# Kernel optimization log

Measured on AMD Instinct MI355X. Metric: run time of the kernel, lower is better.

The kernel has to match this reference:

```python
import jax, jax.numpy as jnp
import numpy as np

N_QUBITS = 12
N_LAYERS = 16
DIM = 1 << N_QUBITS        # 4096
BATCH = 2048
N_CLASS = 5                # Z observables on wires 0..4

# --- static circuit structure (qubit 0 = most significant bit, DeepQuantum order) ---
_idx = np.arange(DIM)

def _cnot_perm(c, t):
    # CNOT(control=c, target=t): flip target bit where control bit is 1
    cbit = 1 << (N_QUBITS - 1 - c)
    tbit = 1 << (N_QUBITS - 1 - t)
    return np.where(_idx & cbit, _idx ^ tbit, _idx)

# cnot_ring: CNOT(q, (q+1) % n) for q = 0..n-1
CNOT_PERMS = [jnp.asarray(_cnot_perm(q, (q + 1) % N_QUBITS)) for q in range(N_QUBITS)]

# <Z_w> sign vectors for wires 0..4, stacked to (N_CLASS, DIM)
Z_SIGNS = jnp.asarray(
    np.stack([1.0 - 2.0 * ((_idx >> (N_QUBITS - 1 - w)) & 1) for w in range(N_CLASS)]).astype(np.float32)
)


def _apply_ry(psi, theta, q):
    """Apply RY(theta) on qubit q to batched state psi of shape (B, DIM)."""
    c = jnp.cos(theta / 2).astype(psi.real.dtype)
    s = jnp.sin(theta / 2).astype(psi.real.dtype)
    b = psi.shape[0]
    psi = psi.reshape(b, 1 << q, 2, 1 << (N_QUBITS - 1 - q))
    p0, p1 = psi[:, :, 0, :], psi[:, :, 1, :]
    out = jnp.stack([c * p0 - s * p1, s * p0 + c * p1], axis=2)
    return out.reshape(b, DIM)


def _circuit(psi, thetas):
    """num_layers x (RY layer + CNOT ring); returns (B, N_CLASS) Z expectations."""
    for l in range(N_LAYERS):
        for q in range(N_QUBITS):
            psi = _apply_ry(psi, thetas[l, q], q)
        for q in range(N_QUBITS):
            psi = psi[:, CNOT_PERMS[q]]
    probs = psi.real * psi.real + psi.imag * psi.imag  # (B, DIM)
    return probs @ Z_SIGNS.T                           # (B, N_CLASS)


def setup_inputs() -> dict:
    key = jax.random.key(0)
    k1, k2, k3, k4 = jax.random.split(key, 4)
    zr = jax.random.normal(k1, (BATCH, DIM), dtype=jnp.float32)
    zi = jax.random.normal(k2, (BATCH, DIM), dtype=jnp.float32)
    norm = jnp.sqrt(jnp.sum(zr * zr + zi * zi, axis=1, keepdims=True))  # valid quantum state
    zr, zi = zr / norm, zi / norm
    thetas = jax.random.normal(k3, (N_LAYERS, N_QUBITS), dtype=jnp.float32)
    y = jax.random.randint(k4, (BATCH,), 0, N_CLASS, dtype=jnp.int64)
    return {"z_real": zr, "z_imag": zi, "thetas": thetas, "y": y}


def reference(z_real, z_imag, thetas, y):
    psi = jax.lax.complex(z_real, z_imag)              # (B, 2**n) complex64
    output = _circuit(psi, thetas)                     # (B, N_CLASS) float32
    logp = jax.nn.log_softmax(output, axis=-1)
    nll = -jnp.take_along_axis(logp, y[:, None].astype(jnp.int32), axis=1)[:, 0]
    loss = jnp.mean(nll)                               # F.cross_entropy(output, y)
    return (loss, output)
```

## Files before the change

kernel.cpp:

```cpp
#include <hip/hip_runtime.h>
#include <math.h>


#define DIM     4096
#define NLAYERS 16
#define BATCH   2048
#define NCLASS  5

typedef float v2f __attribute__((ext_vector_type(2)));

__host__ __device__ constexpr unsigned gperm(unsigned i) {
  for (int q = 11; q >= 0; --q) {
    const unsigned cbit = 1u << (11 - q);
    const unsigned tbit = 1u << (11 - ((q + 1) % 12));
    if (i & cbit) i ^= tbit;
  }
  return i;
}
__host__ __device__ constexpr unsigned Qmap(unsigned lo) {
  return ((lo ^ (lo >> 3)) & 1u) | ((((lo >> 1) ^ (lo >> 3)) & 1u) << 1) |
         (((lo >> 2) & 1u) << 2) | ((lo & 1u) << 3);
}
__host__ __device__ constexpr unsigned Fmap(unsigned x) {
  return (x & 0xF00u) | ((x & 0xFu) << 4) | (((x >> 4) & 0xFu) ^ Qmap(x & 0xFu));
}

#define FOR16(M) M(0) M(1) M(2) M(3) M(4) M(5) M(6) M(7) M(8) M(9) M(10) \
  M(11) M(12) M(13) M(14) M(15)

#define ROT(i, j) {                                          \
    const v2f ti = p##i, tj = p##j;                          \
    p##i = __builtin_elementwise_fma(nkv, tj, ti);           \
    p##j = __builtin_elementwise_fma(kv,  ti, tj); }

#define GM8 ROT(0,8) ROT(1,9) ROT(2,10) ROT(3,11) ROT(4,12) ROT(5,13) \
  ROT(6,14) ROT(7,15)
#define GM4 ROT(0,4) ROT(1,5) ROT(2,6) ROT(3,7) ROT(8,12) ROT(9,13) \
  ROT(10,14) ROT(11,15)
#define GM2 ROT(0,2) ROT(1,3) ROT(4,6) ROT(5,7) ROT(8,10) ROT(9,11) \
  ROT(12,14) ROT(13,15)
#define GM1 ROT(0,1) ROT(2,3) ROT(4,5) ROT(6,7) ROT(8,9) ROT(10,11) \
  ROT(12,13) ROT(14,15)

#define GETK(g) \
  const float kG = __int_as_float(__builtin_amdgcn_readlane( \
      __float_as_int(vkg[(g) & 3]), l + (((g) >> 2) << 4)));

#define DPP8(CTRL, iA,iB,iC,iD,iE,iF,iG,iH) { \
    float a0 = p##iA.x, a1 = p##iA.y, a2 = p##iB.x, a3 = p##iB.y, \
          a4 = p##iC.x, a5 = p##iC.y, a6 = p##iD.x, a7 = p##iD.y, \
          a8 = p##iE.x, a9 = p##iE.y, a10 = p##iF.x, a11 = p##iF.y, \
          a12 = p##iG.x, a13 = p##iG.y, a14 = p##iH.x, a15 = p##iH.y; \
    asm("s_nop 1\n\t" \
        "v_fmac_f32_dpp %0, %0, %16 " CTRL "\n\t" \
        "v_fmac_f32_dpp %1, %1, %16 " CTRL "\n\t" \
        "v_fmac_f32_dpp %2, %2, %16 " CTRL "\n\t" \
        "v_fmac_f32_dpp %3, %3, %16 " CTRL "\n\t" \
        "v_fmac_f32_dpp %4, %4, %16 " CTRL "\n\t" \
        "v_fmac_f32_dpp %5, %5, %16 " CTRL "\n\t" \
        "v_fmac_f32_dpp %6, %6, %16 " CTRL "\n\t" \
        "v_fmac_f32_dpp %7, %7, %16 " CTRL "\n\t" \
        "v_fmac_f32_dpp %8, %8, %16 " CTRL "\n\t" \
        "v_fmac_f32_dpp %9, %9, %16 " CTRL "\n\t" \
        "v_fmac_f32_dpp %10, %10, %16 " CTRL "\n\t" \
        "v_fmac_f32_dpp %11, %11, %16 " CTRL "\n\t" \
        "v_fmac_f32_dpp %12, %12, %16 " CTRL "\n\t" \
        "v_fmac_f32_dpp %13, %13, %16 " CTRL "\n\t" \
        "v_fmac_f32_dpp %14, %14, %16 " CTRL "\n\t" \
        "v_fmac_f32_dpp %15, %15, %16 " CTRL \
        : "+v"(a0), "+v"(a1), "+v"(a2), "+v"(a3), "+v"(a4), "+v"(a5), \
          "+v"(a6), "+v"(a7), "+v"(a8), "+v"(a9), "+v"(a10), "+v"(a11), \
          "+v"(a12), "+v"(a13), "+v"(a14), "+v"(a15) \
        : "v"(sg)); \
    p##iA.x = a0;  p##iA.y = a1;  p##iB.x = a2;  p##iB.y = a3; \
    p##iC.x = a4;  p##iC.y = a5;  p##iD.x = a6;  p##iD.y = a7; \
    p##iE.x = a8;  p##iE.y = a9;  p##iF.x = a10; p##iF.y = a11; \
    p##iG.x = a12; p##iG.y = a13; p##iH.x = a14; p##iH.y = a15; }

#define DPPGATE(CTRL) \
  DPP8(CTRL, 0,1,2,3,4,5,6,7) DPP8(CTRL, 8,9,10,11,12,13,14,15)

__global__ __launch_bounds__(256)
void qnn_sim(const float* __restrict__ zr, const float* __restrict__ zi,
             const float* __restrict__ thetas, const int* __restrict__ y,
             float* __restrict__ out) {
  __shared__ v2f buf2[DIM];
  const int b = blockIdx.x;
  const int t = threadIdx.x;

  const int tn = t ^ (((t >> 2) & 1) * 3);

  const int w1b = ((t & 0xF0) << 4) | (tn & 0xF);
  const int r1b = (int)Fmap((unsigned)t);
  const int Gtn = ((tn << 4) ^ (tn << 3)) & 0xFFF;
  const int r2b = (int)Fmap((unsigned)Gtn);

#define MKADDR(i) \
  const int w1a##i = w1b ^ (int)Fmap((unsigned)i); \
  const int r2a##i = r2b ^ (int)Fmap(gperm((unsigned)i));
  FOR16(MKADDR)
#undef MKADDR

  const bool m7 = ((t ^ (t >> 2)) & 1) != 0;
  const bool m6 = (((t >> 1) ^ (t >> 2)) & 1) != 0;
  const bool m5 = ((t >> 2) & 1) != 0;
  const bool m4 = ((t >> 3) & 1) != 0;

  v2f p0,p1,p2,p3,p4,p5,p6,p7,p8,p9,p10,p11,p12,p13,p14,p15;
  {
    const float4* zr4 = (const float4*)(zr + (size_t)b * DIM + (tn << 4));
    const float4* zi4 = (const float4*)(zi + (size_t)b * DIM + (tn << 4));
    const float4 a0 = zr4[0], a1 = zr4[1], a2 = zr4[2], a3 = zr4[3];
    const float4 b0 = zi4[0], b1 = zi4[1], b2 = zi4[2], b3 = zi4[3];
    p0  = (v2f){a0.x, b0.x}; p1  = (v2f){a0.y, b0.y};
    p2  = (v2f){a0.z, b0.z}; p3  = (v2f){a0.w, b0.w};
    p4  = (v2f){a1.x, b1.x}; p5  = (v2f){a1.y, b1.y};
    p6  = (v2f){a1.z, b1.z}; p7  = (v2f){a1.w, b1.w};
    p8  = (v2f){a2.x, b2.x}; p9  = (v2f){a2.y, b2.y};
    p10 = (v2f){a2.z, b2.z}; p11 = (v2f){a2.w, b2.w};
    p12 = (v2f){a3.x, b3.x}; p13 = (v2f){a3.y, b3.y};
    p14 = (v2f){a3.z, b3.z}; p15 = (v2f){a3.w, b3.w};
  }

  float vkg[4];
  {
    const int lane = t & 63;
    if (lane < 48) {
      const int lsrc = lane & 15;
      const int gb = (lane >> 4) << 2;
#pragma unroll
      for (int j = 0; j < 4; ++j) {
        const float a = 0.5f * thetas[lsrc * 12 + gb + j];
        vkg[j] = sinf(a) / cosf(a);
      }
    } else {
      const int lsrc = lane - 48;
      float c = 1.f;
      for (int g = 0; g < 12; ++g) c *= cosf(0.5f * thetas[lsrc * 12 + g]);
      vkg[0] = c; vkg[1] = 0.f; vkg[2] = 0.f; vkg[3] = 0.f;
    }
  }
  float pcl = 1.f;
#pragma unroll
  for (int l2 = 0; l2 < NLAYERS; ++l2)
    pcl *= __int_as_float(__builtin_amdgcn_readlane(
        __float_as_int(vkg[0]), 48 + l2));
  const float pc2 = pcl * pcl;

#pragma unroll 1
  for (int l = 0; l < NLAYERS; ++l) {
    { GETK(8)  const v2f kv = {kG,kG}, nkv = {-kG,-kG}; GM8 }
    { GETK(9)  const v2f kv = {kG,kG}, nkv = {-kG,-kG}; GM4 }
    { GETK(10) const v2f kv = {kG,kG}, nkv = {-kG,-kG}; GM2 }
    { GETK(11) const v2f kv = {kG,kG}, nkv = {-kG,-kG}; GM1 }

    { GETK(7) const float sg = m7 ? kG : -kG;
      DPPGATE("quad_perm:[1,0,3,2] row_mask:0xf bank_mask:0xf") }
    { GETK(6) const float sg = m6 ? kG : -kG;
      DPPGATE("quad_perm:[2,3,0,1] row_mask:0xf bank_mask:0xf") }
    { GETK(5) const float sg = m5 ? kG : -kG;
      DPPGATE("row_half_mirror row_mask:0xf bank_mask:0xf") }
    { GETK(4) const float sg = m4 ? kG : -kG;
      DPPGATE("row_ror:8 row_mask:0xf bank_mask:0xf") }

    __syncthreads();
#define W1P(i) buf2[w1a##i] = p##i;
    FOR16(W1P)
#undef W1P
    __syncthreads();
#define R1P(i) p##i = buf2[r1b + (i << 8)];
    FOR16(R1P)
#undef R1P

    { GETK(0) const v2f kv = {kG,kG}, nkv = {-kG,-kG}; GM8 }
    { GETK(1) const v2f kv = {kG,kG}, nkv = {-kG,-kG}; GM4 }
    { GETK(2) const v2f kv = {kG,kG}, nkv = {-kG,-kG}; GM2 }
    { GETK(3) const v2f kv = {kG,kG}, nkv = {-kG,-kG}; GM1 }

#define W2P(i) buf2[r1b + (i << 8)] = p##i;
    FOR16(W2P)
#undef W2P
    __syncthreads();
#define R2P(i) p##i = buf2[r2a##i];
    FOR16(R2P)
#undef R2P
  }

  float P = 0.f;
#define ACC(i) P = __builtin_fmaf(p##i.x, p##i.x, P); \
               P = __builtin_fmaf(p##i.y, p##i.y, P);
  FOR16(ACC)
#undef ACC
  P *= pc2;
  float e0 = ((t >> 7) & 1) ? -P : P;
  float e1 = ((t >> 6) & 1) ? -P : P;
  float e2 = ((t >> 5) & 1) ? -P : P;
  float e3 = ((t >> 4) & 1) ? -P : P;
  float e4 = ((t >> 3) & 1) ? -P : P;
#pragma unroll
  for (int off = 32; off >= 1; off >>= 1) {
    e0 += __shfl_xor(e0, off);
    e1 += __shfl_xor(e1, off);
    e2 += __shfl_xor(e2, off);
    e3 += __shfl_xor(e3, off);
    e4 += __shfl_xor(e4, off);
  }
  float* bf = (float*)buf2;
  __syncthreads();
  if ((t & 63) == 0) {
    const int w8 = (t >> 6) * 8;
    bf[w8 + 0] = e0; bf[w8 + 1] = e1; bf[w8 + 2] = e2;
    bf[w8 + 3] = e3; bf[w8 + 4] = e4;
  }
  __syncthreads();
  if (t == 0) {
    const float o0 = bf[0] + bf[8]  + bf[16] + bf[24];
    const float o1 = bf[1] + bf[9]  + bf[17] + bf[25];
    const float o2 = bf[2] + bf[10] + bf[18] + bf[26];
    const float o3 = bf[3] + bf[11] + bf[19] + bf[27];
    const float o4 = bf[4] + bf[12] + bf[20] + bf[28];
    float* op = out + 1 + (size_t)b * NCLASS;
    op[0] = o0; op[1] = o1; op[2] = o2; op[3] = o3; op[4] = o4;
    const float m = fmaxf(fmaxf(fmaxf(o0, o1), fmaxf(o2, o3)), o4);
    const float sum = expf(o0 - m) + expf(o1 - m) + expf(o2 - m) +
                      expf(o3 - m) + expf(o4 - m);
    const int yb = y[b];
    const float oy = (yb == 0) ? o0 : (yb == 1) ? o1 : (yb == 2) ? o2
                   : (yb == 3) ? o3 : o4;
    const float nll = (m + logf(sum)) - oy;
    atomicAdd(out, nll * (1.0f / BATCH));
  }
}

extern "C" void kernel_launch(void* const* d_in, const int* in_sizes, int n_in,
                              void* d_out, int out_size, void* d_ws, size_t ws_size,
                              hipStream_t stream) {
  const float* zr = (const float*)d_in[0];
  const float* zi = (const float*)d_in[1];
  const float* th = (const float*)d_in[2];
  const int*   y  = (const int*)d_in[3];
  float* out = (float*)d_out;
  hipMemsetAsync(out, 0, sizeof(float), stream);
  qnn_sim<<<BATCH, 256, 0, stream>>>(zr, zi, th, y, out);
}
```

Baseline: 192.5 us.

## Simulate each state with a single wavefront holding 64 amplitudes per lane

Each 4096-amplitude state is now processed by one 64-lane wavefront instead of a 256-thread block. Every lane holds 64 complex amplitudes in registers. Six qubits are applied within a lane, four with DPP, one with ds_swizzle and one with ds_bpermute. The per-layer transpose through LDS drops its block barriers, since only one wave touches the buffer, and the cross-wave reduction at the end is removed. In exchange the kernel needs far more VGPRs per lane, launches fewer threads per CU, and adds 128 LDS-routed permutes per gate for the two cross-row qubits.

```diff
diff --git a/kernel.cpp b/kernel.cpp
--- a/kernel.cpp
+++ b/kernel.cpp
@@ -9,38 +9,50 @@
 
 typedef float v2f __attribute__((ext_vector_type(2)));
 
-__host__ __device__ constexpr unsigned gperm(unsigned i) {
-  for (int q = 11; q >= 0; --q) {
-    const unsigned cbit = 1u << (11 - q);
-    const unsigned tbit = 1u << (11 - ((q + 1) % 12));
-    if (i & cbit) i ^= tbit;
-  }
-  return i;
+__device__ __forceinline__ int mmap(int x) { return x ^ (3 * ((x >> 2) & 1)); }
+
+template<int PAT>
+__device__ __forceinline__ float swzf(float x) {
+  return __int_as_float(__builtin_amdgcn_ds_swizzle(__float_as_int(x), PAT));
 }
-__host__ __device__ constexpr unsigned Qmap(unsigned lo) {
-  return ((lo ^ (lo >> 3)) & 1u) | ((((lo >> 1) ^ (lo >> 3)) & 1u) << 1) |
-         (((lo >> 2) & 1u) << 2) | ((lo & 1u) << 3);
-}
-__host__ __device__ constexpr unsigned Fmap(unsigned x) {
-  return (x & 0xF00u) | ((x & 0xFu) << 4) | (((x >> 4) & 0xFu) ^ Qmap(x & 0xFu));
-}
-
-#define FOR16(M) M(0) M(1) M(2) M(3) M(4) M(5) M(6) M(7) M(8) M(9) M(10) \
-  M(11) M(12) M(13) M(14) M(15)
+
+#define FOR64(M) M(0) M(1) M(2) M(3) M(4) M(5) M(6) M(7) M(8) M(9) \
+ M(10) M(11) M(12) M(13) M(14) M(15) M(16) M(17) M(18) M(19) \
+ M(20) M(21) M(22) M(23) M(24) M(25) M(26) M(27) M(28) M(29) \
+ M(30) M(31) M(32) M(33) M(34) M(35) M(36) M(37) M(38) M(39) \
+ M(40) M(41) M(42) M(43) M(44) M(45) M(46) M(47) M(48) M(49) \
+ M(50) M(51) M(52) M(53) M(54) M(55) M(56) M(57) M(58) M(59) \
+ M(60) M(61) M(62) M(63)
+
+#define PR1(M) M(0,1) M(2,3) M(4,5) M(6,7) M(8,9) M(10,11) M(12,13) M(14,15) \
+ M(16,17) M(18,19) M(20,21) M(22,23) M(24,25) M(26,27) M(28,29) M(30,31) \
+ M(32,33) M(34,35) M(36,37) M(38,39) M(40,41) M(42,43) M(44,45) M(46,47) \
+ M(48,49) M(50,51) M(52,53) M(54,55) M(56,57) M(58,59) M(60,61) M(62,63)
+#define PR2(M) M(0,2) M(1,3) M(4,6) M(5,7) M(8,10) M(9,11) M(12,14) M(13,15) \
+ M(16,18) M(17,19) M(20,22) M(21,23) M(24,26) M(25,27) M(28,30) M(29,31) \
+ M(32,34) M(33,35) M(36,38) M(37,39) M(40,42) M(41,43) M(44,46) M(45,47) \
+ M(48,50) M(49,51) M(52,54) M(53,55) M(56,58) M(57,59) M(60,62) M(61,63)
+#define PR4(M) M(0,4) M(1,5) M(2,6) M(3,7) M(8,12) M(9,13) M(10,14) M(11,15) \
+ M(16,20) M(17,21) M(18,22) M(19,23) M(24,28) M(25,29) M(26,30) M(27,31) \
+ M(32,36) M(33,37) M(34,38) M(35,39) M(40,44) M(41,45) M(42,46) M(43,47) \
+ M(48,52) M(49,53) M(50,54) M(51,55) M(56,60) M(57,61) M(58,62) M(59,63)
+#define PR8(M) M(0,8) M(1,9) M(2,10) M(3,11) M(4,12) M(5,13) M(6,14) M(7,15) \
+ M(16,24) M(17,25) M(18,26) M(19,27) M(20,28) M(21,29) M(22,30) M(23,31) \
+ M(32,40) M(33,41) M(34,42) M(35,43) M(36,44) M(37,45) M(38,46) M(39,47) \
+ M(48,56) M(49,57) M(50,58) M(51,59) M(52,60) M(53,61) M(54,62) M(55,63)
+#define PR16(M) M(0,16) M(1,17) M(2,18) M(3,19) M(4,20) M(5,21) M(6,22) M(7,23) \
+ M(8,24) M(9,25) M(10,26) M(11,27) M(12,28) M(13,29) M(14,30) M(15,31) \
+ M(32,48) M(33,49) M(34,50) M(35,51) M(36,52) M(37,53) M(38,54) M(39,55) \
+ M(40,56) M(41,57) M(42,58) M(43,59) M(44,60) M(45,61) M(46,62) M(47,63)
+#define PR32(M) M(0,32) M(1,33) M(2,34) M(3,35) M(4,36) M(5,37) M(6,38) M(7,39) \
+ M(8,40) M(9,41) M(10,42) M(11,43) M(12,44) M(13,45) M(14,46) M(15,47) \
+ M(16,48) M(17,49) M(18,50) M(19,51) M(20,52) M(21,53) M(22,54) M(23,55) \
+ M(24,56) M(25,57) M(26,58) M(27,59) M(28,60) M(29,61) M(30,62) M(31,63)
 
 #define ROT(i, j) {                                          \
     const v2f ti = p##i, tj = p##j;                          \
     p##i = __builtin_elementwise_fma(nkv, tj, ti);           \
     p##j = __builtin_elementwise_fma(kv,  ti, tj); }
-
-#define GM8 ROT(0,8) ROT(1,9) ROT(2,10) ROT(3,11) ROT(4,12) ROT(5,13) \
-  ROT(6,14) ROT(7,15)
-#define GM4 ROT(0,4) ROT(1,5) ROT(2,6) ROT(3,7) ROT(8,12) ROT(9,13) \
-  ROT(10,14) ROT(11,15)
-#define GM2 ROT(0,2) ROT(1,3) ROT(4,6) ROT(5,7) ROT(8,10) ROT(9,11) \
-  ROT(12,14) ROT(13,15)
-#define GM1 ROT(0,1) ROT(2,3) ROT(4,5) ROT(6,7) ROT(8,9) ROT(10,11) \
-  ROT(12,13) ROT(14,15)
 
 #define GETK(g) \
   const float kG = __int_as_float(__builtin_amdgcn_readlane( \
@@ -78,9 +90,12 @@
     p##iG.x = a12; p##iG.y = a13; p##iH.x = a14; p##iH.y = a15; }
 
 #define DPPGATE(CTRL) \
-  DPP8(CTRL, 0,1,2,3,4,5,6,7) DPP8(CTRL, 8,9,10,11,12,13,14,15)
-
-__global__ __launch_bounds__(256)
+  DPP8(CTRL, 0,1,2,3,4,5,6,7) DPP8(CTRL, 8,9,10,11,12,13,14,15) \
+  DPP8(CTRL, 16,17,18,19,20,21,22,23) DPP8(CTRL, 24,25,26,27,28,29,30,31) \
+  DPP8(CTRL, 32,33,34,35,36,37,38,39) DPP8(CTRL, 40,41,42,43,44,45,46,47) \
+  DPP8(CTRL, 48,49,50,51,52,53,54,55) DPP8(CTRL, 56,57,58,59,60,61,62,63)
+
+__global__ __launch_bounds__(64)
 void qnn_sim(const float* __restrict__ zr, const float* __restrict__ zi,
              const float* __restrict__ thetas, const int* __restrict__ y,
              float* __restrict__ out) {
@@ -88,53 +103,55 @@
   const int b = blockIdx.x;
   const int t = threadIdx.x;
 
-  const int tn = t ^ (((t >> 2) & 1) * 3);
-
-  const int w1b = ((t & 0xF0) << 4) | (tn & 0xF);
-  const int r1b = (int)Fmap((unsigned)t);
-  const int Gtn = ((tn << 4) ^ (tn << 3)) & 0xFFF;
-  const int r2b = (int)Fmap((unsigned)Gtn);
-
-#define MKADDR(i) \
-  const int w1a##i = w1b ^ (int)Fmap((unsigned)i); \
-  const int r2a##i = r2b ^ (int)Fmap(gperm((unsigned)i));
-  FOR16(MKADDR)
-#undef MKADDR
-
-  const bool m7 = ((t ^ (t >> 2)) & 1) != 0;
-  const bool m6 = (((t >> 1) ^ (t >> 2)) & 1) != 0;
-  const bool m5 = ((t >> 2) & 1) != 0;
-  const bool m4 = ((t >> 3) & 1) != 0;
-
-  v2f p0,p1,p2,p3,p4,p5,p6,p7,p8,p9,p10,p11,p12,p13,p14,p15;
+  const int n  = mmap(t);
+  const int n0 = n & 1;
+  const int nn = n ^ (n >> 1);
+  const int nnm = mmap(nn);
+
+  const int rb00 = (n0 << 11) | nnm;
+  const int rb10 = (n0 << 11) | (nnm ^ 0x30);
+  const int rb01 = ((n0 ^ 1) << 11) | nnm;
+  const int rb11 = ((n0 ^ 1) << 11) | (nnm ^ 0x30);
+
+  const int bpaddr = (t ^ 32) << 2;
+
+  const bool s5 = ((t ^ (t >> 2)) & 1) != 0;
+  const bool s4 = (((t >> 1) ^ (t >> 2)) & 1) != 0;
+  const bool s3 = ((t >> 2) & 1) != 0;
+  const bool s2 = ((t >> 3) & 1) != 0;
+  const bool s1 = ((t >> 4) & 1) != 0;
+  const bool s0 = ((t >> 5) & 1) != 0;
+
+  v2f p0,p1,p2,p3,p4,p5,p6,p7,p8,p9,p10,p11,p12,p13,p14,p15,
+      p16,p17,p18,p19,p20,p21,p22,p23,p24,p25,p26,p27,p28,p29,p30,p31,
+      p32,p33,p34,p35,p36,p37,p38,p39,p40,p41,p42,p43,p44,p45,p46,p47,
+      p48,p49,p50,p51,p52,p53,p54,p55,p56,p57,p58,p59,p60,p61,p62,p63;
+
   {
-    const float4* zr4 = (const float4*)(zr + (size_t)b * DIM + (tn << 4));
-    const float4* zi4 = (const float4*)(zi + (size_t)b * DIM + (tn << 4));
-    const float4 a0 = zr4[0], a1 = zr4[1], a2 = zr4[2], a3 = zr4[3];
-    const float4 b0 = zi4[0], b1 = zi4[1], b2 = zi4[2], b3 = zi4[3];
-    p0  = (v2f){a0.x, b0.x}; p1  = (v2f){a0.y, b0.y};
-    p2  = (v2f){a0.z, b0.z}; p3  = (v2f){a0.w, b0.w};
-    p4  = (v2f){a1.x, b1.x}; p5  = (v2f){a1.y, b1.y};
-    p6  = (v2f){a1.z, b1.z}; p7  = (v2f){a1.w, b1.w};
-    p8  = (v2f){a2.x, b2.x}; p9  = (v2f){a2.y, b2.y};
-    p10 = (v2f){a2.z, b2.z}; p11 = (v2f){a2.w, b2.w};
-    p12 = (v2f){a3.x, b3.x}; p13 = (v2f){a3.y, b3.y};
-    p14 = (v2f){a3.z, b3.z}; p15 = (v2f){a3.w, b3.w};
+    const float4* zr4 = (const float4*)(zr + (size_t)b * DIM + (n << 6));
+    const float4* zi4 = (const float4*)(zi + (size_t)b * DIM + (n << 6));
+#define LDJ(j,A,B,C,D) { const float4 a = zr4[j]; const float4 c = zi4[j]; \
+    p##A = (v2f){a.x, c.x}; p##B = (v2f){a.y, c.y}; \
+    p##C = (v2f){a.z, c.z}; p##D = (v2f){a.w, c.w}; }
+    LDJ(0,0,1,2,3)     LDJ(1,4,5,6,7)     LDJ(2,8,9,10,11)   LDJ(3,12,13,14,15)
+    LDJ(4,16,17,18,19) LDJ(5,20,21,22,23) LDJ(6,24,25,26,27) LDJ(7,28,29,30,31)
+    LDJ(8,32,33,34,35) LDJ(9,36,37,38,39) LDJ(10,40,41,42,43) LDJ(11,44,45,46,47)
+    LDJ(12,48,49,50,51) LDJ(13,52,53,54,55) LDJ(14,56,57,58,59) LDJ(15,60,61,62,63)
+#undef LDJ
   }
 
   float vkg[4];
   {
-    const int lane = t & 63;
-    if (lane < 48) {
-      const int lsrc = lane & 15;
-      const int gb = (lane >> 4) << 2;
+    if (t < 48) {
+      const int lsrc = t & 15;
+      const int gb = (t >> 4) << 2;
 #pragma unroll
       for (int j = 0; j < 4; ++j) {
         const float a = 0.5f * thetas[lsrc * 12 + gb + j];
         vkg[j] = sinf(a) / cosf(a);
       }
     } else {
-      const int lsrc = lane - 48;
+      const int lsrc = t - 48;
       float c = 1.f;
       for (int g = 0; g < 12; ++g) c *= cosf(0.5f * thetas[lsrc * 12 + g]);
       vkg[0] = c; vkg[1] = 0.f; vkg[2] = 0.f; vkg[3] = 0.f;
@@ -149,54 +166,66 @@
 
 #pragma unroll 1
   for (int l = 0; l < NLAYERS; ++l) {
-    { GETK(8)  const v2f kv = {kG,kG}, nkv = {-kG,-kG}; GM8 }
-    { GETK(9)  const v2f kv = {kG,kG}, nkv = {-kG,-kG}; GM4 }
-    { GETK(10) const v2f kv = {kG,kG}, nkv = {-kG,-kG}; GM2 }
-    { GETK(11) const v2f kv = {kG,kG}, nkv = {-kG,-kG}; GM1 }
-
-    { GETK(7) const float sg = m7 ? kG : -kG;
+    { GETK(5) const float sg = s5 ? kG : -kG;
       DPPGATE("quad_perm:[1,0,3,2] row_mask:0xf bank_mask:0xf") }
-    { GETK(6) const float sg = m6 ? kG : -kG;
+    { GETK(4) const float sg = s4 ? kG : -kG;
       DPPGATE("quad_perm:[2,3,0,1] row_mask:0xf bank_mask:0xf") }
-    { GETK(5) const float sg = m5 ? kG : -kG;
+    { GETK(3) const float sg = s3 ? kG : -kG;
       DPPGATE("row_half_mirror row_mask:0xf bank_mask:0xf") }
-    { GETK(4) const float sg = m4 ? kG : -kG;
+    { GETK(2) const float sg = s2 ? kG : -kG;
       DPPGATE("row_ror:8 row_mask:0xf bank_mask:0xf") }
 
-    __syncthreads();
-#define W1P(i) buf2[w1a##i] = p##i;
-    FOR16(W1P)
-#undef W1P
-    __syncthreads();
-#define R1P(i) p##i = buf2[r1b + (i << 8)];
-    FOR16(R1P)
-#undef R1P
-
-    { GETK(0) const v2f kv = {kG,kG}, nkv = {-kG,-kG}; GM8 }
-    { GETK(1) const v2f kv = {kG,kG}, nkv = {-kG,-kG}; GM4 }
-    { GETK(2) const v2f kv = {kG,kG}, nkv = {-kG,-kG}; GM2 }
-    { GETK(3) const v2f kv = {kG,kG}, nkv = {-kG,-kG}; GM1 }
-
-#define W2P(i) buf2[r1b + (i << 8)] = p##i;
-    FOR16(W2P)
-#undef W2P
-    __syncthreads();
-#define R2P(i) p##i = buf2[r2a##i];
-    FOR16(R2P)
-#undef R2P
+    {
+      GETK(1)
+      const float sg = s1 ? kG : -kG;
+      const v2f skv = {sg, sg};
+#define SWG(i) { v2f pr; pr.x = swzf<0x401F>(p##i.x); pr.y = swzf<0x401F>(p##i.y); \
+      p##i = __builtin_elementwise_fma(skv, pr, p##i); }
+      FOR64(SWG)
+#undef SWG
+    }
+
+    {
+      GETK(0)
+      const float sg = s0 ? kG : -kG;
+      const v2f skv = {sg, sg};
+#define BPG(i) { v2f pr; \
+      pr.x = __int_as_float(__builtin_amdgcn_ds_bpermute(bpaddr, __float_as_int(p##i.x))); \
+      pr.y = __int_as_float(__builtin_amdgcn_ds_bpermute(bpaddr, __float_as_int(p##i.y))); \
+      p##i = __builtin_elementwise_fma(skv, pr, p##i); }
+      FOR64(BPG)
+#undef BPG
+    }
+
+    { GETK(11) const v2f kv = {kG,kG}, nkv = {-kG,-kG}; PR1(ROT) }
+    { GETK(10) const v2f kv = {kG,kG}, nkv = {-kG,-kG}; PR2(ROT) }
+    { GETK(9)  const v2f kv = {kG,kG}, nkv = {-kG,-kG}; PR4(ROT) }
+    { GETK(8)  const v2f kv = {kG,kG}, nkv = {-kG,-kG}; PR8(ROT) }
+    { GETK(7)  const v2f kv = {kG,kG}, nkv = {-kG,-kG}; PR16(ROT) }
+    { GETK(6)  const v2f kv = {kG,kG}, nkv = {-kG,-kG}; PR32(ROT) }
+
+#define TW(i) buf2[((i) << 6) + t] = p##i;
+    FOR64(TW)
+#undef TW
+    asm volatile("" ::: "memory");
+#define TR(i) p##i = buf2[(((i) & 1) ? (((i) & 32) ? rb11 : rb10) \
+                                     : (((i) & 32) ? rb01 : rb00)) \
+                          + (((((i) ^ ((i) >> 1)) & 31)) << 6)];
+    FOR64(TR)
+#undef TR
   }
 
   float P = 0.f;
 #define ACC(i) P = __builtin_fmaf(p##i.x, p##i.x, P); \
                P = __builtin_fmaf(p##i.y, p##i.y, P);
-  FOR16(ACC)
+  FOR64(ACC)
 #undef ACC
   P *= pc2;
-  float e0 = ((t >> 7) & 1) ? -P : P;
-  float e1 = ((t >> 6) & 1) ? -P : P;
-  float e2 = ((t >> 5) & 1) ? -P : P;
-  float e3 = ((t >> 4) & 1) ? -P : P;
-  float e4 = ((t >> 3) & 1) ? -P : P;
+  float e0 = s0 ? -P : P;
+  float e1 = s1 ? -P : P;
+  float e2 = s2 ? -P : P;
+  float e3 = s3 ? -P : P;
+  float e4 = s4 ? -P : P;
 #pragma unroll
   for (int off = 32; off >= 1; off >>= 1) {
     e0 += __shfl_xor(e0, off);
@@ -205,28 +234,15 @@
     e3 += __shfl_xor(e3, off);
     e4 += __shfl_xor(e4, off);
   }
-  float* bf = (float*)buf2;
-  __syncthreads();
-  if ((t & 63) == 0) {
-    const int w8 = (t >> 6) * 8;
-    bf[w8 + 0] = e0; bf[w8 + 1] = e1; bf[w8 + 2] = e2;
-    bf[w8 + 3] = e3; bf[w8 + 4] = e4;
-  }
-  __syncthreads();
   if (t == 0) {
-    const float o0 = bf[0] + bf[8]  + bf[16] + bf[24];
-    const float o1 = bf[1] + bf[9]  + bf[17] + bf[25];
-    const float o2 = bf[2] + bf[10] + bf[18] + bf[26];
-    const float o3 = bf[3] + bf[11] + bf[19] + bf[27];
-    const float o4 = bf[4] + bf[12] + bf[20] + bf[28];
     float* op = out + 1 + (size_t)b * NCLASS;
-    op[0] = o0; op[1] = o1; op[2] = o2; op[3] = o3; op[4] = o4;
-    const float m = fmaxf(fmaxf(fmaxf(o0, o1), fmaxf(o2, o3)), o4);
-    const float sum = expf(o0 - m) + expf(o1 - m) + expf(o2 - m) +
-                      expf(o3 - m) + expf(o4 - m);
+    op[0] = e0; op[1] = e1; op[2] = e2; op[3] = e3; op[4] = e4;
+    const float m = fmaxf(fmaxf(fmaxf(e0, e1), fmaxf(e2, e3)), e4);
+    const float sum = expf(e0 - m) + expf(e1 - m) + expf(e2 - m) +
+                      expf(e3 - m) + expf(e4 - m);
     const int yb = y[b];
-    const float oy = (yb == 0) ? o0 : (yb == 1) ? o1 : (yb == 2) ? o2
-                   : (yb == 3) ? o3 : o4;
+    const float oy = (yb == 0) ? e0 : (yb == 1) ? e1 : (yb == 2) ? e2
+                   : (yb == 3) ? e3 : e4;
     const float nll = (m + logf(sum)) - oy;
     atomicAdd(out, nll * (1.0f / BATCH));
   }
@@ -241,5 +257,5 @@
   const int*   y  = (const int*)d_in[3];
   float* out = (float*)d_out;
   hipMemsetAsync(out, 0, sizeof(float), stream);
-  qnn_sim<<<BATCH, 256, 0, stream>>>(zr, zi, th, y, out);
+  qnn_sim<<<BATCH, 64, 0, stream>>>(zr, zi, th, y, out);
 }
```

After: 308.2 us. 1.6x slower.

## Halve shared-memory buffer with two-phase exchanges to raise occupancy

Applied to the files above, without the earlier changes.

The 4096-entry complex shared buffer (32 KB) is cut to 2048 entries, and each of the two per-layer all-to-all exchanges is split into two half-sized phases with extra barriers and temporary registers. Launch bounds now request 8 blocks per CU so that more blocks can be resident and hide latency. In exchange it doubles the barrier count per exchange (from 2 to 6 per layer), adds divergent branches on the thread half, and raises register pressure from the temporaries, which could hurt if occupancy was not the limiter.

```diff
diff --git a/kernel.cpp b/kernel.cpp
--- a/kernel.cpp
+++ b/kernel.cpp
@@ -6,6 +6,7 @@
 #define NLAYERS 16
 #define BATCH   2048
 #define NCLASS  5
+#define HMSK    0x7FF
 
 typedef float v2f __attribute__((ext_vector_type(2)));
 
@@ -24,6 +25,9 @@
 __host__ __device__ constexpr unsigned Fmap(unsigned x) {
   return (x & 0xF00u) | ((x & 0xFu) << 4) | (((x >> 4) & 0xFu) ^ Qmap(x & 0xFu));
 }
+
+#define W1C(i) ((int)Fmap((unsigned)(i)))
+#define R2C(i) ((int)(Fmap(gperm((unsigned)(i))) & HMSK))
 
 #define FOR16(M) M(0) M(1) M(2) M(3) M(4) M(5) M(6) M(7) M(8) M(9) M(10) \
   M(11) M(12) M(13) M(14) M(15)
@@ -80,26 +84,22 @@
 #define DPPGATE(CTRL) \
   DPP8(CTRL, 0,1,2,3,4,5,6,7) DPP8(CTRL, 8,9,10,11,12,13,14,15)
 
-__global__ __launch_bounds__(256)
+__global__ __launch_bounds__(256, 8)
 void qnn_sim(const float* __restrict__ zr, const float* __restrict__ zi,
              const float* __restrict__ thetas, const int* __restrict__ y,
              float* __restrict__ out) {
-  __shared__ v2f buf2[DIM];
+  __shared__ v2f buf2[2048];
   const int b = blockIdx.x;
   const int t = threadIdx.x;
 
   const int tn = t ^ (((t >> 2) & 1) * 3);
 
-  const int w1b = ((t & 0xF0) << 4) | (tn & 0xF);
-  const int r1b = (int)Fmap((unsigned)t);
-  const int Gtn = ((tn << 4) ^ (tn << 3)) & 0xFFF;
-  const int r2b = (int)Fmap((unsigned)Gtn);
-
-#define MKADDR(i) \
-  const int w1a##i = w1b ^ (int)Fmap((unsigned)i); \
-  const int r2a##i = r2b ^ (int)Fmap(gperm((unsigned)i));
-  FOR16(MKADDR)
-#undef MKADDR
+  const int w1bm = ((((t & 0xF0) << 4) | (tn & 0xF)) & HMSK);
+  const int r1b  = (int)Fmap((unsigned)t);
+  const int Gtn  = ((tn << 4) ^ (tn << 3)) & 0xFFF;
+  const int r2bm = (int)(Fmap((unsigned)Gtn) & HMSK);
+
+  const bool wlo = (t < 128);
 
   const bool m7 = ((t ^ (t >> 2)) & 1) != 0;
   const bool m6 = (((t >> 1) ^ (t >> 2)) & 1) != 0;
@@ -107,6 +107,7 @@
   const bool m4 = ((t >> 3) & 1) != 0;
 
   v2f p0,p1,p2,p3,p4,p5,p6,p7,p8,p9,p10,p11,p12,p13,p14,p15;
+  v2f tv0,tv1,tv2,tv3,tv4,tv5,tv6,tv7;
   {
     const float4* zr4 = (const float4*)(zr + (size_t)b * DIM + (tn << 4));
     const float4* zi4 = (const float4*)(zi + (size_t)b * DIM + (tn << 4));
@@ -153,7 +154,6 @@
     { GETK(9)  const v2f kv = {kG,kG}, nkv = {-kG,-kG}; GM4 }
     { GETK(10) const v2f kv = {kG,kG}, nkv = {-kG,-kG}; GM2 }
     { GETK(11) const v2f kv = {kG,kG}, nkv = {-kG,-kG}; GM1 }
-
     { GETK(7) const float sg = m7 ? kG : -kG;
       DPPGATE("quad_perm:[1,0,3,2] row_mask:0xf bank_mask:0xf") }
     { GETK(6) const float sg = m6 ? kG : -kG;
@@ -164,26 +164,82 @@
       DPPGATE("row_ror:8 row_mask:0xf bank_mask:0xf") }
 
     __syncthreads();
-#define W1P(i) buf2[w1a##i] = p##i;
-    FOR16(W1P)
+    if (wlo) {
+#define W1P(i) buf2[w1bm ^ W1C(i)] = p##i;
+      FOR16(W1P)
 #undef W1P
-    __syncthreads();
-#define R1P(i) p##i = buf2[r1b + (i << 8)];
-    FOR16(R1P)
-#undef R1P
+    }
+    __syncthreads();
+    if (!wlo) { tv0=p0; tv1=p1; tv2=p2; tv3=p3;
+                tv4=p4; tv5=p5; tv6=p6; tv7=p7; }
+    p0 = buf2[r1b];          p1 = buf2[r1b + 256];
+    p2 = buf2[r1b + 512];    p3 = buf2[r1b + 768];
+    p4 = buf2[r1b + 1024];   p5 = buf2[r1b + 1280];
+    p6 = buf2[r1b + 1536];   p7 = buf2[r1b + 1792];
+    __syncthreads();
+    if (!wlo) {
+      buf2[w1bm ^ W1C(0)] = tv0; buf2[w1bm ^ W1C(1)] = tv1;
+      buf2[w1bm ^ W1C(2)] = tv2; buf2[w1bm ^ W1C(3)] = tv3;
+      buf2[w1bm ^ W1C(4)] = tv4; buf2[w1bm ^ W1C(5)] = tv5;
+      buf2[w1bm ^ W1C(6)] = tv6; buf2[w1bm ^ W1C(7)] = tv7;
+      buf2[w1bm ^ W1C(8)]  = p8;  buf2[w1bm ^ W1C(9)]  = p9;
+      buf2[w1bm ^ W1C(10)] = p10; buf2[w1bm ^ W1C(11)] = p11;
+      buf2[w1bm ^ W1C(12)] = p12; buf2[w1bm ^ W1C(13)] = p13;
+      buf2[w1bm ^ W1C(14)] = p14; buf2[w1bm ^ W1C(15)] = p15;
+    }
+    __syncthreads();
+    p8  = buf2[r1b];         p9  = buf2[r1b + 256];
+    p10 = buf2[r1b + 512];   p11 = buf2[r1b + 768];
+    p12 = buf2[r1b + 1024];  p13 = buf2[r1b + 1280];
+    p14 = buf2[r1b + 1536];  p15 = buf2[r1b + 1792];
 
     { GETK(0) const v2f kv = {kG,kG}, nkv = {-kG,-kG}; GM8 }
     { GETK(1) const v2f kv = {kG,kG}, nkv = {-kG,-kG}; GM4 }
     { GETK(2) const v2f kv = {kG,kG}, nkv = {-kG,-kG}; GM2 }
     { GETK(3) const v2f kv = {kG,kG}, nkv = {-kG,-kG}; GM1 }
 
-#define W2P(i) buf2[r1b + (i << 8)] = p##i;
-    FOR16(W2P)
-#undef W2P
-    __syncthreads();
-#define R2P(i) p##i = buf2[r2a##i];
-    FOR16(R2P)
-#undef R2P
+    buf2[r1b]        = p0;  buf2[r1b + 256]  = p1;
+    buf2[r1b + 512]  = p2;  buf2[r1b + 768]  = p3;
+    buf2[r1b + 1024] = p4;  buf2[r1b + 1280] = p5;
+    buf2[r1b + 1536] = p6;  buf2[r1b + 1792] = p7;
+    if (wlo) { tv0 = p8;  tv1 = p10; tv2 = p12; tv3 = p14; }
+    else     { tv0 = p9;  tv1 = p11; tv2 = p13; tv3 = p15; }
+    __syncthreads();
+    if (wlo) {
+      p0  = buf2[r2bm ^ R2C(0)];  p2  = buf2[r2bm ^ R2C(2)];
+      p4  = buf2[r2bm ^ R2C(4)];  p6  = buf2[r2bm ^ R2C(6)];
+      p8  = buf2[r2bm ^ R2C(8)];  p10 = buf2[r2bm ^ R2C(10)];
+      p12 = buf2[r2bm ^ R2C(12)]; p14 = buf2[r2bm ^ R2C(14)];
+    } else {
+      p1  = buf2[r2bm ^ R2C(1)];  p3  = buf2[r2bm ^ R2C(3)];
+      p5  = buf2[r2bm ^ R2C(5)];  p7  = buf2[r2bm ^ R2C(7)];
+      p9  = buf2[r2bm ^ R2C(9)];  p11 = buf2[r2bm ^ R2C(11)];
+      p13 = buf2[r2bm ^ R2C(13)]; p15 = buf2[r2bm ^ R2C(15)];
+    }
+    __syncthreads();
+    if (wlo) {
+      buf2[r1b]        = tv0; buf2[r1b + 256]  = p9;
+      buf2[r1b + 512]  = tv1; buf2[r1b + 768]  = p11;
+      buf2[r1b + 1024] = tv2; buf2[r1b + 1280] = p13;
+      buf2[r1b + 1536] = tv3; buf2[r1b + 1792] = p15;
+    } else {
+      buf2[r1b]        = p8;  buf2[r1b + 256]  = tv0;
+      buf2[r1b + 512]  = p10; buf2[r1b + 768]  = tv1;
+      buf2[r1b + 1024] = p12; buf2[r1b + 1280] = tv2;
+      buf2[r1b + 1536] = p14; buf2[r1b + 1792] = tv3;
+    }
+    __syncthreads();
+    if (wlo) {
+      p1  = buf2[r2bm ^ R2C(1)];  p3  = buf2[r2bm ^ R2C(3)];
+      p5  = buf2[r2bm ^ R2C(5)];  p7  = buf2[r2bm ^ R2C(7)];
+      p9  = buf2[r2bm ^ R2C(9)];  p11 = buf2[r2bm ^ R2C(11)];
+      p13 = buf2[r2bm ^ R2C(13)]; p15 = buf2[r2bm ^ R2C(15)];
+    } else {
+      p0  = buf2[r2bm ^ R2C(0)];  p2  = buf2[r2bm ^ R2C(2)];
+      p4  = buf2[r2bm ^ R2C(4)];  p6  = buf2[r2bm ^ R2C(6)];
+      p8  = buf2[r2bm ^ R2C(8)];  p10 = buf2[r2bm ^ R2C(10)];
+      p12 = buf2[r2bm ^ R2C(12)]; p14 = buf2[r2bm ^ R2C(14)];
+    }
   }
 
   float P = 0.f;
```

Measured after the change: 443.2 us. 130% more time.

## Process two batch states per block with software-pipelined gate/transpose overlap

Applied to the files above, without the earlier changes.

Each block now simulates two batch samples with two register sets and two LDS buffers. The layer loop is skewed so that one state's register gates run while the other state's LDS transposes are in flight, hiding barrier and LDS latency behind ALU work. The grid is halved. The cost is roughly double the register and LDS use per block, which may lower occupancy or cause spills, and more complex control flow at the pipeline boundaries.

```diff
diff --git a/kernel.cpp b/kernel.cpp
--- a/kernel.cpp
+++ b/kernel.cpp
@@ -25,32 +25,32 @@
   return (x & 0xF00u) | ((x & 0xFu) << 4) | (((x >> 4) & 0xFu) ^ Qmap(x & 0xFu));
 }
 
-#define FOR16(M) M(0) M(1) M(2) M(3) M(4) M(5) M(6) M(7) M(8) M(9) M(10) \
-  M(11) M(12) M(13) M(14) M(15)
-
-#define ROT(i, j) {                                          \
-    const v2f ti = p##i, tj = p##j;                          \
-    p##i = __builtin_elementwise_fma(nkv, tj, ti);           \
-    p##j = __builtin_elementwise_fma(kv,  ti, tj); }
-
-#define GM8 ROT(0,8) ROT(1,9) ROT(2,10) ROT(3,11) ROT(4,12) ROT(5,13) \
-  ROT(6,14) ROT(7,15)
-#define GM4 ROT(0,4) ROT(1,5) ROT(2,6) ROT(3,7) ROT(8,12) ROT(9,13) \
-  ROT(10,14) ROT(11,15)
-#define GM2 ROT(0,2) ROT(1,3) ROT(4,6) ROT(5,7) ROT(8,10) ROT(9,11) \
-  ROT(12,14) ROT(13,15)
-#define GM1 ROT(0,1) ROT(2,3) ROT(4,5) ROT(6,7) ROT(8,9) ROT(10,11) \
-  ROT(12,13) ROT(14,15)
-
-#define GETK(g) \
+#define W1C(i) ((int)Fmap((unsigned)(i)))
+#define R2C(i) ((int)Fmap(gperm((unsigned)(i))))
+
+#define ROT(P, i, j) {                                        \
+    const v2f ti = P##i, tj = P##j;                           \
+    P##i = __builtin_elementwise_fma(nkv, tj, ti);            \
+    P##j = __builtin_elementwise_fma(kv,  ti, tj); }
+
+#define GM8(P) ROT(P,0,8) ROT(P,1,9) ROT(P,2,10) ROT(P,3,11) ROT(P,4,12) \
+  ROT(P,5,13) ROT(P,6,14) ROT(P,7,15)
+#define GM4(P) ROT(P,0,4) ROT(P,1,5) ROT(P,2,6) ROT(P,3,7) ROT(P,8,12) \
+  ROT(P,9,13) ROT(P,10,14) ROT(P,11,15)
+#define GM2(P) ROT(P,0,2) ROT(P,1,3) ROT(P,4,6) ROT(P,5,7) ROT(P,8,10) \
+  ROT(P,9,11) ROT(P,12,14) ROT(P,13,15)
+#define GM1(P) ROT(P,0,1) ROT(P,2,3) ROT(P,4,5) ROT(P,6,7) ROT(P,8,9) \
+  ROT(P,10,11) ROT(P,12,13) ROT(P,14,15)
+
+#define GETKL(g, LL) \
   const float kG = __int_as_float(__builtin_amdgcn_readlane( \
-      __float_as_int(vkg[(g) & 3]), l + (((g) >> 2) << 4)));
-
-#define DPP8(CTRL, iA,iB,iC,iD,iE,iF,iG,iH) { \
-    float a0 = p##iA.x, a1 = p##iA.y, a2 = p##iB.x, a3 = p##iB.y, \
-          a4 = p##iC.x, a5 = p##iC.y, a6 = p##iD.x, a7 = p##iD.y, \
-          a8 = p##iE.x, a9 = p##iE.y, a10 = p##iF.x, a11 = p##iF.y, \
-          a12 = p##iG.x, a13 = p##iG.y, a14 = p##iH.x, a15 = p##iH.y; \
+      __float_as_int(vkg[(g) & 3]), (LL) + (((g) >> 2) << 4)));
+
+#define DPP8(P, CTRL, iA,iB,iC,iD,iE,iF,iG,iH) { \
+    float a0 = P##iA.x, a1 = P##iA.y, a2 = P##iB.x, a3 = P##iB.y, \
+          a4 = P##iC.x, a5 = P##iC.y, a6 = P##iD.x, a7 = P##iD.y, \
+          a8 = P##iE.x, a9 = P##iE.y, a10 = P##iF.x, a11 = P##iF.y, \
+          a12 = P##iG.x, a13 = P##iG.y, a14 = P##iH.x, a15 = P##iH.y; \
     asm("s_nop 1\n\t" \
         "v_fmac_f32_dpp %0, %0, %16 " CTRL "\n\t" \
         "v_fmac_f32_dpp %1, %1, %16 " CTRL "\n\t" \
@@ -72,55 +72,100 @@
           "+v"(a6), "+v"(a7), "+v"(a8), "+v"(a9), "+v"(a10), "+v"(a11), \
           "+v"(a12), "+v"(a13), "+v"(a14), "+v"(a15) \
         : "v"(sg)); \
-    p##iA.x = a0;  p##iA.y = a1;  p##iB.x = a2;  p##iB.y = a3; \
-    p##iC.x = a4;  p##iC.y = a5;  p##iD.x = a6;  p##iD.y = a7; \
-    p##iE.x = a8;  p##iE.y = a9;  p##iF.x = a10; p##iF.y = a11; \
-    p##iG.x = a12; p##iG.y = a13; p##iH.x = a14; p##iH.y = a15; }
-
-#define DPPGATE(CTRL) \
-  DPP8(CTRL, 0,1,2,3,4,5,6,7) DPP8(CTRL, 8,9,10,11,12,13,14,15)
+    P##iA.x = a0;  P##iA.y = a1;  P##iB.x = a2;  P##iB.y = a3; \
+    P##iC.x = a4;  P##iC.y = a5;  P##iD.x = a6;  P##iD.y = a7; \
+    P##iE.x = a8;  P##iE.y = a9;  P##iF.x = a10; P##iF.y = a11; \
+    P##iG.x = a12; P##iG.y = a13; P##iH.x = a14; P##iH.y = a15; }
+
+#define DPPGATE(P, CTRL) \
+  DPP8(P, CTRL, 0,1,2,3,4,5,6,7) DPP8(P, CTRL, 8,9,10,11,12,13,14,15)
+
+#define L1GATES(P, LL) \
+  { GETKL(8,LL)  const v2f kv={kG,kG}, nkv={-kG,-kG}; GM8(P) } \
+  { GETKL(9,LL)  const v2f kv={kG,kG}, nkv={-kG,-kG}; GM4(P) } \
+  { GETKL(10,LL) const v2f kv={kG,kG}, nkv={-kG,-kG}; GM2(P) } \
+  { GETKL(11,LL) const v2f kv={kG,kG}, nkv={-kG,-kG}; GM1(P) } \
+  { GETKL(7,LL) const float sg = m7 ? kG : -kG; \
+    DPPGATE(P, "quad_perm:[1,0,3,2] row_mask:0xf bank_mask:0xf") } \
+  { GETKL(6,LL) const float sg = m6 ? kG : -kG; \
+    DPPGATE(P, "quad_perm:[2,3,0,1] row_mask:0xf bank_mask:0xf") } \
+  { GETKL(5,LL) const float sg = m5 ? kG : -kG; \
+    DPPGATE(P, "row_half_mirror row_mask:0xf bank_mask:0xf") } \
+  { GETKL(4,LL) const float sg = m4 ? kG : -kG; \
+    DPPGATE(P, "row_ror:8 row_mask:0xf bank_mask:0xf") }
+
+#define L2GATES(P, LL) \
+  { GETKL(0,LL) const v2f kv={kG,kG}, nkv={-kG,-kG}; GM8(P) } \
+  { GETKL(1,LL) const v2f kv={kG,kG}, nkv={-kG,-kG}; GM4(P) } \
+  { GETKL(2,LL) const v2f kv={kG,kG}, nkv={-kG,-kG}; GM2(P) } \
+  { GETKL(3,LL) const v2f kv={kG,kG}, nkv={-kG,-kG}; GM1(P) }
+
+#define W1S(P,B,i) B[w1b ^ W1C(i)] = P##i;
+#define TRIP1W(P,B) W1S(P,B,0) W1S(P,B,1) W1S(P,B,2) W1S(P,B,3) W1S(P,B,4) \
+  W1S(P,B,5) W1S(P,B,6) W1S(P,B,7) W1S(P,B,8) W1S(P,B,9) W1S(P,B,10) \
+  W1S(P,B,11) W1S(P,B,12) W1S(P,B,13) W1S(P,B,14) W1S(P,B,15)
+#define R1S(P,B,i) P##i = B[r1b + ((i) << 8)];
+#define TRIP1R(P,B) R1S(P,B,0) R1S(P,B,1) R1S(P,B,2) R1S(P,B,3) R1S(P,B,4) \
+  R1S(P,B,5) R1S(P,B,6) R1S(P,B,7) R1S(P,B,8) R1S(P,B,9) R1S(P,B,10) \
+  R1S(P,B,11) R1S(P,B,12) R1S(P,B,13) R1S(P,B,14) R1S(P,B,15)
+#define W2S(P,B,i) B[r1b + ((i) << 8)] = P##i;
+#define TRIP2W(P,B) W2S(P,B,0) W2S(P,B,1) W2S(P,B,2) W2S(P,B,3) W2S(P,B,4) \
+  W2S(P,B,5) W2S(P,B,6) W2S(P,B,7) W2S(P,B,8) W2S(P,B,9) W2S(P,B,10) \
+  W2S(P,B,11) W2S(P,B,12) W2S(P,B,13) W2S(P,B,14) W2S(P,B,15)
+#define R2S(P,B,i) P##i = B[r2b ^ R2C(i)];
+#define TRIP2R(P,B) R2S(P,B,0) R2S(P,B,1) R2S(P,B,2) R2S(P,B,3) R2S(P,B,4) \
+  R2S(P,B,5) R2S(P,B,6) R2S(P,B,7) R2S(P,B,8) R2S(P,B,9) R2S(P,B,10) \
+  R2S(P,B,11) R2S(P,B,12) R2S(P,B,13) R2S(P,B,14) R2S(P,B,15)
+
+#define ACC1(P, i, V) \
+  V = __builtin_fmaf(P##i.x, P##i.x, V); \
+  V = __builtin_fmaf(P##i.y, P##i.y, V);
+#define ACC16(P, V) \
+  ACC1(P,0,V) ACC1(P,1,V) ACC1(P,2,V) ACC1(P,3,V) \
+  ACC1(P,4,V) ACC1(P,5,V) ACC1(P,6,V) ACC1(P,7,V) \
+  ACC1(P,8,V) ACC1(P,9,V) ACC1(P,10,V) ACC1(P,11,V) \
+  ACC1(P,12,V) ACC1(P,13,V) ACC1(P,14,V) ACC1(P,15,V)
+
+#define LOADSTATE(P, SRCR, SRCI) { \
+    const float4* zr4 = (const float4*)(SRCR); \
+    const float4* zi4 = (const float4*)(SRCI); \
+    const float4 a0 = zr4[0], a1 = zr4[1], a2 = zr4[2], a3 = zr4[3]; \
+    const float4 b0 = zi4[0], b1 = zi4[1], b2 = zi4[2], b3 = zi4[3]; \
+    P##0  = (v2f){a0.x, b0.x}; P##1  = (v2f){a0.y, b0.y}; \
+    P##2  = (v2f){a0.z, b0.z}; P##3  = (v2f){a0.w, b0.w}; \
+    P##4  = (v2f){a1.x, b1.x}; P##5  = (v2f){a1.y, b1.y}; \
+    P##6  = (v2f){a1.z, b1.z}; P##7  = (v2f){a1.w, b1.w}; \
+    P##8  = (v2f){a2.x, b2.x}; P##9  = (v2f){a2.y, b2.y}; \
+    P##10 = (v2f){a2.z, b2.z}; P##11 = (v2f){a2.w, b2.w}; \
+    P##12 = (v2f){a3.x, b3.x}; P##13 = (v2f){a3.y, b3.y}; \
+    P##14 = (v2f){a3.z, b3.z}; P##15 = (v2f){a3.w, b3.w}; }
 
 __global__ __launch_bounds__(256)
 void qnn_sim(const float* __restrict__ zr, const float* __restrict__ zi,
              const float* __restrict__ thetas, const int* __restrict__ y,
              float* __restrict__ out) {
-  __shared__ v2f buf2[DIM];
+  __shared__ v2f bufA[DIM];
+  __shared__ v2f bufB[DIM];
   const int b = blockIdx.x;
+  const int sA = 2 * b, sB = 2 * b + 1;
   const int t = threadIdx.x;
 
   const int tn = t ^ (((t >> 2) & 1) * 3);
-
   const int w1b = ((t & 0xF0) << 4) | (tn & 0xF);
   const int r1b = (int)Fmap((unsigned)t);
   const int Gtn = ((tn << 4) ^ (tn << 3)) & 0xFFF;
   const int r2b = (int)Fmap((unsigned)Gtn);
 
-#define MKADDR(i) \
-  const int w1a##i = w1b ^ (int)Fmap((unsigned)i); \
-  const int r2a##i = r2b ^ (int)Fmap(gperm((unsigned)i));
-  FOR16(MKADDR)
-#undef MKADDR
-
   const bool m7 = ((t ^ (t >> 2)) & 1) != 0;
   const bool m6 = (((t >> 1) ^ (t >> 2)) & 1) != 0;
   const bool m5 = ((t >> 2) & 1) != 0;
   const bool m4 = ((t >> 3) & 1) != 0;
 
-  v2f p0,p1,p2,p3,p4,p5,p6,p7,p8,p9,p10,p11,p12,p13,p14,p15;
-  {
-    const float4* zr4 = (const float4*)(zr + (size_t)b * DIM + (tn << 4));
-    const float4* zi4 = (const float4*)(zi + (size_t)b * DIM + (tn << 4));
-    const float4 a0 = zr4[0], a1 = zr4[1], a2 = zr4[2], a3 = zr4[3];
-    const float4 b0 = zi4[0], b1 = zi4[1], b2 = zi4[2], b3 = zi4[3];
-    p0  = (v2f){a0.x, b0.x}; p1  = (v2f){a0.y, b0.y};
-    p2  = (v2f){a0.z, b0.z}; p3  = (v2f){a0.w, b0.w};
-    p4  = (v2f){a1.x, b1.x}; p5  = (v2f){a1.y, b1.y};
-    p6  = (v2f){a1.z, b1.z}; p7  = (v2f){a1.w, b1.w};
-    p8  = (v2f){a2.x, b2.x}; p9  = (v2f){a2.y, b2.y};
-    p10 = (v2f){a2.z, b2.z}; p11 = (v2f){a2.w, b2.w};
-    p12 = (v2f){a3.x, b3.x}; p13 = (v2f){a3.y, b3.y};
-    p14 = (v2f){a3.z, b3.z}; p15 = (v2f){a3.w, b3.w};
-  }
+  v2f pA0,pA1,pA2,pA3,pA4,pA5,pA6,pA7,pA8,pA9,pA10,pA11,pA12,pA13,pA14,pA15;
+  v2f pB0,pB1,pB2,pB3,pB4,pB5,pB6,pB7,pB8,pB9,pB10,pB11,pB12,pB13,pB14,pB15;
+
+  LOADSTATE(pA, zr + (size_t)sA * DIM + (tn << 4), zi + (size_t)sA * DIM + (tn << 4))
+  LOADSTATE(pB, zr + (size_t)sB * DIM + (tn << 4), zi + (size_t)sB * DIM + (tn << 4))
 
   float vkg[4];
   {
@@ -147,70 +192,64 @@
         __float_as_int(vkg[0]), 48 + l2));
   const float pc2 = pcl * pcl;
 
+  L1GATES(pB, 0)
+  TRIP1W(pB, bufB)
+  __syncthreads();
+  TRIP1R(pB, bufB)
+  L2GATES(pB, 0)
+
 #pragma unroll 1
   for (int l = 0; l < NLAYERS; ++l) {
-    { GETK(8)  const v2f kv = {kG,kG}, nkv = {-kG,-kG}; GM8 }
-    { GETK(9)  const v2f kv = {kG,kG}, nkv = {-kG,-kG}; GM4 }
-    { GETK(10) const v2f kv = {kG,kG}, nkv = {-kG,-kG}; GM2 }
-    { GETK(11) const v2f kv = {kG,kG}, nkv = {-kG,-kG}; GM1 }
-
-    { GETK(7) const float sg = m7 ? kG : -kG;
-      DPPGATE("quad_perm:[1,0,3,2] row_mask:0xf bank_mask:0xf") }
-    { GETK(6) const float sg = m6 ? kG : -kG;
-      DPPGATE("quad_perm:[2,3,0,1] row_mask:0xf bank_mask:0xf") }
-    { GETK(5) const float sg = m5 ? kG : -kG;
-      DPPGATE("row_half_mirror row_mask:0xf bank_mask:0xf") }
-    { GETK(4) const float sg = m4 ? kG : -kG;
-      DPPGATE("row_ror:8 row_mask:0xf bank_mask:0xf") }
-
+    const bool more = (l < NLAYERS - 1);
+    TRIP2W(pB, bufB)
+    L1GATES(pA, l)
     __syncthreads();
-#define W1P(i) buf2[w1a##i] = p##i;
-    FOR16(W1P)
-#undef W1P
+    TRIP2R(pB, bufB)
+    TRIP1W(pA, bufA)
+    if (more) { L1GATES(pB, l + 1) }
     __syncthreads();
-#define R1P(i) p##i = buf2[r1b + (i << 8)];
-    FOR16(R1P)
-#undef R1P
-
-    { GETK(0) const v2f kv = {kG,kG}, nkv = {-kG,-kG}; GM8 }
-    { GETK(1) const v2f kv = {kG,kG}, nkv = {-kG,-kG}; GM4 }
-    { GETK(2) const v2f kv = {kG,kG}, nkv = {-kG,-kG}; GM2 }
-    { GETK(3) const v2f kv = {kG,kG}, nkv = {-kG,-kG}; GM1 }
-
-#define W2P(i) buf2[r1b + (i << 8)] = p##i;
-    FOR16(W2P)
-#undef W2P
+    TRIP1R(pA, bufA)
+    if (more) { TRIP1W(pB, bufB) }
+    L2GATES(pA, l)
     __syncthreads();
-#define R2P(i) p##i = buf2[r2a##i];
-    FOR16(R2P)
-#undef R2P
-  }
-
-  float P = 0.f;
-#define ACC(i) P = __builtin_fmaf(p##i.x, p##i.x, P); \
-               P = __builtin_fmaf(p##i.y, p##i.y, P);
-  FOR16(ACC)
-#undef ACC
-  P *= pc2;
-  float e0 = ((t >> 7) & 1) ? -P : P;
-  float e1 = ((t >> 6) & 1) ? -P : P;
-  float e2 = ((t >> 5) & 1) ? -P : P;
-  float e3 = ((t >> 4) & 1) ? -P : P;
-  float e4 = ((t >> 3) & 1) ? -P : P;
+    if (more) { TRIP1R(pB, bufB) }
+    TRIP2W(pA, bufA)
+    if (more) { L2GATES(pB, l + 1) }
+    __syncthreads();
+    TRIP2R(pA, bufA)
+  }
+
+  float PA = 0.f, PB = 0.f;
+  ACC16(pA, PA)
+  ACC16(pB, PB)
+  PA *= pc2;
+  PB *= pc2;
+  const float sg0 = ((t >> 7) & 1) ? -1.f : 1.f;
+  const float sg1 = ((t >> 6) & 1) ? -1.f : 1.f;
+  const float sg2 = ((t >> 5) & 1) ? -1.f : 1.f;
+  const float sg3 = ((t >> 4) & 1) ? -1.f : 1.f;
+  const float sg4 = ((t >> 3) & 1) ? -1.f : 1.f;
+  float eA0 = sg0 * PA, eA1 = sg1 * PA, eA2 = sg2 * PA,
+        eA3 = sg3 * PA, eA4 = sg4 * PA;
+  float eB0 = sg0 * PB, eB1 = sg1 * PB, eB2 = sg2 * PB,
+        eB3 = sg3 * PB, eB4 = sg4 * PB;
 #pragma unroll
   for (int off = 32; off >= 1; off >>= 1) {
-    e0 += __shfl_xor(e0, off);
-    e1 += __shfl_xor(e1, off);
-    e2 += __shfl_xor(e2, off);
-    e3 += __shfl_xor(e3, off);
-    e4 += __shfl_xor(e4, off);
-  }
-  float* bf = (float*)buf2;
+    eA0 += __shfl_xor(eA0, off); eA1 += __shfl_xor(eA1, off);
+    eA2 += __shfl_xor(eA2, off); eA3 += __shfl_xor(eA3, off);
+    eA4 += __shfl_xor(eA4, off);
+    eB0 += __shfl_xor(eB0, off); eB1 += __shfl_xor(eB1, off);
+    eB2 += __shfl_xor(eB2, off); eB3 += __shfl_xor(eB3, off);
+    eB4 += __shfl_xor(eB4, off);
+  }
+  float* bf = (float*)bufA;
   __syncthreads();
   if ((t & 63) == 0) {
     const int w8 = (t >> 6) * 8;
-    bf[w8 + 0] = e0; bf[w8 + 1] = e1; bf[w8 + 2] = e2;
-    bf[w8 + 3] = e3; bf[w8 + 4] = e4;
+    bf[w8 + 0] = eA0; bf[w8 + 1] = eA1; bf[w8 + 2] = eA2;
+    bf[w8 + 3] = eA3; bf[w8 + 4] = eA4;
+    bf[32 + w8 + 0] = eB0; bf[32 + w8 + 1] = eB1; bf[32 + w8 + 2] = eB2;
+    bf[32 + w8 + 3] = eB3; bf[32 + w8 + 4] = eB4;
   }
   __syncthreads();
   if (t == 0) {
@@ -219,12 +258,29 @@
     const float o2 = bf[2] + bf[10] + bf[18] + bf[26];
     const float o3 = bf[3] + bf[11] + bf[19] + bf[27];
     const float o4 = bf[4] + bf[12] + bf[20] + bf[28];
-    float* op = out + 1 + (size_t)b * NCLASS;
+    float* op = out + 1 + (size_t)sA * NCLASS;
     op[0] = o0; op[1] = o1; op[2] = o2; op[3] = o3; op[4] = o4;
     const float m = fmaxf(fmaxf(fmaxf(o0, o1), fmaxf(o2, o3)), o4);
     const float sum = expf(o0 - m) + expf(o1 - m) + expf(o2 - m) +
                       expf(o3 - m) + expf(o4 - m);
-    const int yb = y[b];
+    const int yb = y[sA];
+    const float oy = (yb == 0) ? o0 : (yb == 1) ? o1 : (yb == 2) ? o2
+                   : (yb == 3) ? o3 : o4;
+    const float nll = (m + logf(sum)) - oy;
+    atomicAdd(out, nll * (1.0f / BATCH));
+  }
+  if (t == 64) {
+    const float o0 = bf[32+0] + bf[32+8]  + bf[32+16] + bf[32+24];
+    const float o1 = bf[32+1] + bf[32+9]  + bf[32+17] + bf[32+25];
+    const float o2 = bf[32+2] + bf[32+10] + bf[32+18] + bf[32+26];
+    const float o3 = bf[32+3] + bf[32+11] + bf[32+19] + bf[32+27];
+    const float o4 = bf[32+4] + bf[32+12] + bf[32+20] + bf[32+28];
+    float* op = out + 1 + (size_t)sB * NCLASS;
+    op[0] = o0; op[1] = o1; op[2] = o2; op[3] = o3; op[4] = o4;
+    const float m = fmaxf(fmaxf(fmaxf(o0, o1), fmaxf(o2, o3)), o4);
+    const float sum = expf(o0 - m) + expf(o1 - m) + expf(o2 - m) +
+                      expf(o3 - m) + expf(o4 - m);
+    const int yb = y[sB];
     const float oy = (yb == 0) ? o0 : (yb == 1) ? o1 : (yb == 2) ? o2
                    : (yb == 3) ? o3 : o4;
     const float nll = (m + logf(sum)) - oy;
@@ -241,5 +297,5 @@
   const int*   y  = (const int*)d_in[3];
   float* out = (float*)d_out;
   hipMemsetAsync(out, 0, sizeof(float), stream);
-  qnn_sim<<<BATCH, 256, 0, stream>>>(zr, zi, th, y, out);
-}
+  qnn_sim<<<BATCH / 2, 256, 0, stream>>>(zr, zi, th, y, out);
+}
```

Result: slower. 224.0 us (+16.3%).
